# Performance work log

Hardware: AMD Instinct MI355X
Metric: run time of the kernel (lower is better)

The kernel has to match this reference:

```python
import math
import jax
import jax.numpy as jnp
import numpy as np
from jax import lax

Q = 64          # num_quantiles (init default)
EPS = 1e-8      # eps (init default)


def setup_inputs() -> dict:
    key = jax.random.key(0)
    B, T, C = 64, 4096, 128
    x = jax.random.normal(key, (B, T, C), dtype=jnp.float32)
    return {"x": x}


def _build_quantile_table(x):
    """x: (B,T,C) -> quantiles (B,C,Q), levels (Q,). Unmasked branch."""
    B, T, C = x.shape
    levels = jnp.linspace(0.5 / Q, 1.0 - 0.5 / Q, Q, dtype=x.dtype)
    x_sorted = jnp.sort(x, axis=1)                      # (B,T,C) sorted over time
    positions = jnp.clip(levels * T - 0.5, 0.0, float(T - 1))   # (Q,)
    pos_int = jnp.clip(positions.astype(jnp.int32), 0, T - 2)   # (Q,)
    pos_frac = jnp.clip(positions - pos_int.astype(x.dtype), 0.0, 1.0)
    x_bct = jnp.transpose(x_sorted, (0, 2, 1))          # (B,C,T)
    q0 = x_bct[..., pos_int]                            # (B,C,Q)
    q1 = x_bct[..., jnp.minimum(pos_int + 1, T - 1)]    # (B,C,Q)
    quantiles = q0 * (1.0 - pos_frac) + q1 * pos_frac
    return quantiles, levels


def _interp_cdf(x_bc, q_bc, levels):
    """Piecewise-linear F_X(x): x_bc (N,T), q_bc (N,Q) monotone, levels (Q,)."""
    # batched searchsorted (right) per row
    idx = jax.vmap(lambda a, v: jnp.searchsorted(a, v, side="right"))(q_bc, x_bc)
    idx = jnp.clip(idx, 1, Q - 1)                       # (N,T)
    x0 = jnp.take_along_axis(q_bc, idx - 1, axis=-1)
    x1 = jnp.take_along_axis(q_bc, idx, axis=-1)
    y0 = levels[idx - 1]
    y1 = levels[idx]
    slope = (y1 - y0) / jnp.maximum(x1 - x0, 1e-12)
    return y0 + slope * (x_bc - x0)


def _probit(p):
    p_safe = jnp.clip(p, 1e-6, 1.0 - 1e-6)
    return jax.scipy.special.erfinv(2.0 * p_safe - 1.0) * math.sqrt(2.0)


def reference(x):
    B, T, C = x.shape
    quantiles, levels = _build_quantile_table(x)
    # torch detaches the quantile table: gradients flow through x only
    quantiles = lax.stop_gradient(quantiles)
    x_bc = jnp.transpose(x, (0, 2, 1)).reshape(B * C, T)
    q_bc = quantiles.reshape(B * C, Q)
    p_bc = jnp.clip(_interp_cdf(x_bc, q_bc, levels), EPS, 1.0 - EPS)
    z_bc = _probit(p_bc)
    return jnp.transpose(z_bc.reshape(B, C, T), (0, 2, 1))
```

## Files before the change

### kernel.cpp

```cpp
#include <hip/hip_runtime.h>
#include <math.h>

#define BB 64
#define TT 4096
#define CC 128
#define NQ 64
#define TCH2 128
#define NBKT 2048
#define NBKT_G 1024

__global__ __launch_bounds__(256) void transpose_kernel(const float* __restrict__ x,
                                                        float* __restrict__ xT) {
    __shared__ float tile[64][65];
    const int cb = blockIdx.x;
    const int tb = blockIdx.y;
    const int b  = blockIdx.z;
    const int tid = threadIdx.x;
    const int q = tid >> 6;
    const int l = tid & 63;

    const float* xs = x + ((size_t)b * TT + (size_t)tb * 64) * CC + (size_t)cb * 64;
    #pragma unroll
    for (int j = 0; j < 16; ++j) {
        int tl = q * 16 + j;
        tile[tl][l] = xs[(size_t)tl * CC + l];
    }
    __syncthreads();
    float* xd = xT + ((size_t)b * CC + (size_t)cb * 64) * TT + (size_t)tb * 64;
    #pragma unroll
    for (int j = 0; j < 16; ++j) {
        int cl = q * 16 + j;
        xd[(size_t)cl * TT + l] = tile[l][cl];
    }
}

__global__ __launch_bounds__(256) void bucket_quantile_T(const float* __restrict__ xT,
                                                         float* __restrict__ qtab) {
    __shared__ unsigned       A[NBKT];
    __shared__ unsigned short cum16[NBKT + 2];
    __shared__ unsigned char  flag8[NBKT];
    __shared__ unsigned short rankinfo[128];
    __shared__ unsigned short pb16[132];
    __shared__ unsigned       cur2[132];
    __shared__ unsigned       wsum[4], wsum2[4];

    const int row = blockIdx.x;
    const float* xrow = xT + (size_t)row * TT;
    const int tid = threadIdx.x, lane = tid & 63, wid = tid >> 6;

    float vv[16];
    #pragma unroll
    for (int j = 0; j < 4; ++j) {
        float4 v4 = ((const float4*)xrow)[j * 256 + tid];
        vv[j * 4 + 0] = v4.x; vv[j * 4 + 1] = v4.y;
        vv[j * 4 + 2] = v4.z; vv[j * 4 + 3] = v4.w;
    }

    *(uint4*)&A[tid * 8]      = make_uint4(0u, 0u, 0u, 0u);
    *(uint4*)&A[tid * 8 + 4]  = make_uint4(0u, 0u, 0u, 0u);
    *(uint2*)&flag8[tid * 8]  = make_uint2(~0u, ~0u);
    __syncthreads();

    #pragma unroll
    for (int j = 0; j < 16; ++j) {
        int bk = (int)((vv[j] + 5.0f) * 204.8f);
        bk = bk < 0 ? 0 : (bk > NBKT - 1 ? NBKT - 1 : bk);
        atomicAdd(&A[bk], 1u);
    }
    __syncthreads();

    uint4 h0 = *(uint4*)&A[tid * 8];
    uint4 h1 = *(uint4*)&A[tid * 8 + 4];
    unsigned S = h0.x + h0.y + h0.z + h0.w + h1.x + h1.y + h1.z + h1.w;
    unsigned incl = S;
    #pragma unroll
    for (int off = 1; off < 64; off <<= 1) {
        unsigned n = __shfl_up(incl, off, 64);
        if (lane >= off) incl += n;
    }
    if (lane == 63) wsum[wid] = incl;
    __syncthreads();
    unsigned base = incl - S;
    for (int w = 0; w < wid; ++w) base += wsum[w];

    unsigned carr[9];
    carr[0] = base;
    carr[1] = carr[0] + h0.x; carr[2] = carr[1] + h0.y;
    carr[3] = carr[2] + h0.z; carr[4] = carr[3] + h0.w;
    carr[5] = carr[4] + h1.x; carr[6] = carr[5] + h1.y;
    carr[7] = carr[6] + h1.z; carr[8] = carr[7] + h1.w;
    #pragma unroll
    for (int bi = 0; bi < 8; ++bi)
        cum16[tid * 8 + bi] = (unsigned short)carr[bi];
    if (tid == 255) cum16[NBKT] = (unsigned short)TT;

    unsigned flg = 0, myLen = 0, myCnt = 0;
    #pragma unroll
    for (int bi = 0; bi < 8; ++bi) {
        const int cs = (int)carr[bi], ce = (int)carr[bi + 1];
        if (ce > cs) {
            int t0 = cs - 32;
            int q0 = t0 < 0 ? 0 : (t0 >> 6);
            int q1 = (ce >> 6); if (q1 > 63) q1 = 63;
            bool any = false;
            for (int q = q0; q <= q1; ++q) {
                int r1 = (q << 6) + 31, r2 = r1 + 1;
                bool i1 = (r1 >= cs) && (r1 < ce);
                bool i2 = (r2 >= cs) && (r2 < ce);
                if (i1) rankinfo[2 * q]     = (unsigned short)(tid * 8 + bi);
                if (i2) rankinfo[2 * q + 1] = (unsigned short)(tid * 8 + bi);
                any |= (i1 || i2);
            }
            if (any) { flg |= (1u << bi); myLen += (unsigned)(ce - cs); myCnt++; }
        }
    }

    unsigned pk = (myLen << 16) | myCnt;
    unsigned incl2 = pk;
    #pragma unroll
    for (int off = 1; off < 64; off <<= 1) {
        unsigned n = __shfl_up(incl2, off, 64);
        if (lane >= off) incl2 += n;
    }
    if (lane == 63) wsum2[wid] = incl2;
    __syncthreads();
    unsigned b2 = incl2 - pk;
    for (int w = 0; w < wid; ++w) b2 += wsum2[w];
    unsigned lenB = b2 >> 16, cntB = b2 & 0xFFFFu;
    #pragma unroll
    for (int bi = 0; bi < 8; ++bi) {
        if (flg & (1u << bi)) {
            int s = tid * 8 + bi;
            flag8[s] = (unsigned char)cntB;
            pb16[cntB] = (unsigned short)lenB;
            cur2[cntB] = lenB;
            cntB++;
            lenB += carr[bi + 1] - carr[bi];
        }
    }
    __syncthreads();

    #pragma unroll
    for (int j = 0; j < 16; ++j) {
        int bk = (int)((vv[j] + 5.0f) * 204.8f);
        bk = bk < 0 ? 0 : (bk > NBKT - 1 ? NBKT - 1 : bk);
        unsigned char fl = flag8[bk];
        if (fl != 0xFFu) {
            unsigned p = atomicAdd(&cur2[fl], 1u);
            if (p < (unsigned)NBKT) ((float*)A)[p] = vv[j];
        }
    }
    __syncthreads();

    if (tid < 128) {
        const int j = tid;
        const int r = ((j >> 1) << 6) + 31 + (j & 1);
        const int s = rankinfo[j];
        const int cs = (int)cum16[s];
        const int L = (int)cum16[s + 1] - cs;
        const int k = r - cs;
        const unsigned char fid = flag8[s];
        const float* seg = (const float*)A + pb16[fid];

        float ans = 0.0f;
        for (int i = 0; i < L; ++i) {
            float vi = seg[i];
            int rk = 0;
            for (int jj = 0; jj < L; ++jj) {
                float vj = seg[jj];
                rk += (vj < vi) || (vj == vi && jj < i);
            }
            if (rk == k) { ans = vi; break; }
        }
        float vo = __shfl_xor(ans, 1, 64);
        if ((tid & 1) == 0)
            qtab[(size_t)row * NQ + (j >> 1)] = (ans + vo) * 0.5f;
    }
}

__global__ __launch_bounds__(256) void bucket_quantile_G(const float* __restrict__ x,
                                                         float* __restrict__ qtab) {
    __shared__ unsigned hist[NBKT_G];
    __shared__ unsigned cum[NBKT_G];
    __shared__ unsigned cur[NBKT_G];
    __shared__ float    pool[TT];
    __shared__ unsigned wsum[4];

    const int bid = blockIdx.x;
    const int row = ((bid & 7) << 10) | (bid >> 3);
    const int b = row >> 7, c = row & (CC - 1);
    const float* xrow = x + (size_t)b * TT * CC + c;
    const int tid = threadIdx.x;
    const int lane = tid & 63, wid = tid >> 6;

    float vv[16];
    #pragma unroll
    for (int j = 0; j < 16; ++j)
        vv[j] = xrow[(size_t)((j << 8) + tid) * CC];

    *(uint4*)&hist[tid << 2] = make_uint4(0u, 0u, 0u, 0u);
    __syncthreads();

    #pragma unroll
    for (int j = 0; j < 16; ++j) {
        int bk = (int)((vv[j] + 5.0f) * 102.4f);
        bk = bk < 0 ? 0 : (bk > NBKT_G - 1 ? NBKT_G - 1 : bk);
        atomicAdd(&hist[bk], 1u);
    }
    __syncthreads();

    uint4 h = *(uint4*)&hist[tid << 2];
    unsigned S = h.x + h.y + h.z + h.w;
    unsigned incl = S;
    #pragma unroll
    for (int off = 1; off < 64; off <<= 1) {
        unsigned n = __shfl_up(incl, off, 64);
        if (lane >= off) incl += n;
    }
    if (lane == 63) wsum[wid] = incl;
    __syncthreads();
    unsigned base = incl - S;
    for (int w = 0; w < wid; ++w) base += wsum[w];
    {
        unsigned c0 = base, c1 = c0 + h.x, c2 = c1 + h.y, c3 = c2 + h.z;
        *(uint4*)&cum[tid << 2] = make_uint4(c0, c1, c2, c3);
        *(uint4*)&cur[tid << 2] = make_uint4(c0, c1, c2, c3);
    }
    __syncthreads();

    #pragma unroll
    for (int j = 0; j < 16; ++j) {
        int bk = (int)((vv[j] + 5.0f) * 102.4f);
        bk = bk < 0 ? 0 : (bk > NBKT_G - 1 ? NBKT_G - 1 : bk);
        unsigned p = atomicAdd(&cur[bk], 1u);
        pool[p] = vv[j];
    }
    __syncthreads();

    if (tid < 128) {
        const int q = tid >> 1;
        const int r = (q << 6) + 31 + (tid & 1);
        int pos = 0;
        #pragma unroll
        for (int step = 512; step >= 1; step >>= 1) {
            int np = pos + step;
            if (np <= NBKT_G - 1 && (int)cum[np] <= r) pos = np;
        }
        const int segbase = (int)cum[pos];
        const int L = (int)hist[pos];
        const int k = r - segbase;
        const float* seg = &pool[segbase];

        float ans = 0.0f;
        for (int i = 0; i < L; ++i) {
            float vi = seg[i];
            int rk = 0;
            for (int jj = 0; jj < L; ++jj) {
                float vj = seg[jj];
                rk += (vj < vi) || (vj == vi && jj < i);
            }
            if (rk == k) { ans = vi; break; }
        }
        float vo = __shfl_xor(ans, 1, 64);
        if ((tid & 1) == 0)
            qtab[(size_t)row * NQ + q] = (ans + vo) * 0.5f;
    }
}

__global__ __launch_bounds__(256) void apply_kernel(const float* __restrict__ x,
                                                    const float* __restrict__ qtab,
                                                    float* __restrict__ out) {
    __shared__ float qtT[NQ][64];
    const int b   = blockIdx.x;
    const int tch = blockIdx.y;
    const int ch  = blockIdx.z;
    const int tid = threadIdx.x;

    const float* qsrc = qtab + ((size_t)b * CC + (size_t)ch * 64) * NQ;
    for (int i = tid; i < 64 * NQ; i += 256) {
        int cl = i >> 6, k = i & 63;
        qtT[k][cl ^ k] = qsrc[i];
    }
    __syncthreads();

    const int myc = tid & 63;
    const int trow0 = tid >> 6;
    const size_t base = (size_t)b * TT * CC + (size_t)tch * TCH2 * CC
                      + (size_t)ch * 64;
    const float* xp = x + base;
    float* op = out + base;
    const float invq = 1.0f / (float)NQ;

    float pv0 = qtT[7][myc ^ 7],   pv1 = qtT[15][myc ^ 15];
    float pv2 = qtT[23][myc ^ 23], pv3 = qtT[31][myc ^ 31];
    float pv4 = qtT[39][myc ^ 39], pv5 = qtT[47][myc ^ 47];
    float pv6 = qtT[55][myc ^ 55];

    #pragma unroll
    for (int g = 0; g < 4; ++g) {
        float v[8];
        int   pos[8];
        int   off[8];
        #pragma unroll
        for (int e = 0; e < 8; ++e) {
            int t = trow0 + 4 * (g * 8 + e);
            off[e] = t * CC + myc;
            v[e] = xp[off[e]];
        }

        #pragma unroll
        for (int e = 0; e < 8; ++e) {
            int p = (pv3 <= v[e]) ? 32 : 0;
            float p16 = (p == 0) ? pv1 : pv5;
            p += (p16 <= v[e]) ? 16 : 0;
            float p8 = (p == 0) ? pv0 : (p == 16) ? pv2 : (p == 32) ? pv4 : pv6;
            p += (p8 <= v[e]) ? 8 : 0;
            pos[e] = p;
        }

        #pragma unroll
        for (int step = 4; step >= 1; step >>= 1) {
            float pr[8];
            #pragma unroll
            for (int e = 0; e < 8; ++e) {
                int np = pos[e] + step - 1;
                pr[e] = qtT[np][myc ^ np];
            }
            #pragma unroll
            for (int e = 0; e < 8; ++e)
                if (pr[e] <= v[e]) pos[e] += step;
        }

        float x0[8], x1[8];
        #pragma unroll
        for (int e = 0; e < 8; ++e) {
            int idx = pos[e];
            idx = idx < 1 ? 1 : (idx > NQ - 1 ? NQ - 1 : idx);
            pos[e] = idx;
            x0[e] = qtT[idx - 1][myc ^ (idx - 1)];
            x1[e] = qtT[idx][myc ^ idx];
        }

        #pragma unroll
        for (int e = 0; e < 8; ++e) {
            const float y0 = ((float)pos[e] - 0.5f) * invq;
            const float rcp = __builtin_amdgcn_rcpf(fmaxf(x1[e] - x0[e], 1e-12f));
            float p = fmaf(invq * rcp, v[e] - x0[e], y0);
            p = fminf(fmaxf(p, 1e-6f), 1.0f - 1e-6f);

            const float xx = 2.0f * p - 1.0f;
            float w = -__logf((1.0f - xx) * (1.0f + xx));
            float z;
            if (w < 5.0f) {
                float ww = w - 2.5f;
                z = 2.81022636e-08f;
                z = fmaf(z, ww, 3.43273939e-07f);
                z = fmaf(z, ww, -3.5233877e-06f);
                z = fmaf(z, ww, -4.39150654e-06f);
                z = fmaf(z, ww, 0.00021858087f);
                z = fmaf(z, ww, -0.00125372503f);
                z = fmaf(z, ww, -0.00417768164f);
                z = fmaf(z, ww, 0.246640727f);
                z = fmaf(z, ww, 1.50140941f);
            } else {
                float ww = sqrtf(w) - 3.0f;
                z = -0.000200214257f;
                z = fmaf(z, ww, 0.000100950558f);
                z = fmaf(z, ww, 0.00134934322f);
                z = fmaf(z, ww, -0.00367342844f);
                z = fmaf(z, ww, 0.00573950773f);
                z = fmaf(z, ww, -0.0076224613f);
                z = fmaf(z, ww, 0.00943887047f);
                z = fmaf(z, ww, 1.00167406f);
                z = fmaf(z, ww, 2.83297682f);
            }
            op[off[e]] = z * xx * 1.4142135623730951f;
        }
    }
}

extern "C" void kernel_launch(void* const* d_in, const int* in_sizes, int n_in,
                              void* d_out, int out_size, void* d_ws, size_t ws_size,
                              hipStream_t stream) {
    const float* x = (const float*)d_in[0];
    float* out = (float*)d_out;
    float* qtab = (float*)d_ws;
    const size_t qtab_bytes = (size_t)BB * CC * NQ * 4;
    const size_t xT_bytes   = (size_t)BB * CC * TT * 4;

    if (ws_size >= qtab_bytes + xT_bytes) {
        float* xT = (float*)((char*)d_ws + qtab_bytes);
        dim3 tgrid(2, 64, BB);
        transpose_kernel<<<tgrid, 256, 0, stream>>>(x, xT);
        bucket_quantile_T<<<BB * CC, 256, 0, stream>>>(xT, qtab);
    } else {
        bucket_quantile_G<<<BB * CC, 256, 0, stream>>>(x, qtab);
    }
    dim3 grid(BB, TT / TCH2, 2);
    apply_kernel<<<grid, 256, 0, stream>>>(x, qtab, out);
}
```

Baseline: 213.7 us.

## Process one quantile row per wavefront instead of per block

The bucket-quantile kernel now assigns each row to a single 64-lane wavefront, with four rows per block. Each wave uses its own 1024-bin shared histogram and candidate pool, so block-wide __syncthreads are replaced by wave-local scans and fences. This removes cross-wave barriers and per-row block overhead. In exchange, each lane holds 64 values in registers and the histogram is coarser, which lengthens the brute-force rank selection inside the bins that hold target ranks.

Result: slower. 452.9 us (+111.9%).

```diff
diff --git a/kernel.cpp b/kernel.cpp
--- a/kernel.cpp
+++ b/kernel.cpp
@@ -6,7 +6,8 @@
 #define CC 128
 #define NQ 64
 #define TCH2 128
-#define NBKT 2048
+#define NBW 1024
+#define PCAP 1024
 #define NBKT_G 1024
 
 __global__ __launch_bounds__(256) void transpose_kernel(const float* __restrict__ x,
@@ -34,69 +35,67 @@
     }
 }
 
-__global__ __launch_bounds__(256) void bucket_quantile_T(const float* __restrict__ xT,
+__global__ __launch_bounds__(256) void bucket_quantile_W(const float* __restrict__ xT,
                                                          float* __restrict__ qtab) {
-    __shared__ unsigned       A[NBKT];
-    __shared__ unsigned short cum16[NBKT + 2];
-    __shared__ unsigned char  flag8[NBKT];
-    __shared__ unsigned short rankinfo[128];
-    __shared__ unsigned short pb16[132];
-    __shared__ unsigned       cur2[132];
-    __shared__ unsigned       wsum[4], wsum2[4];
-
-    const int row = blockIdx.x;
+    __shared__ unsigned       histW[4][NBW];
+    __shared__ float          poolW[4][PCAP];
+    __shared__ unsigned       rankW[4][128];
+    __shared__ unsigned       curW[4][132];
+    __shared__ unsigned short pbW[4][132];
+    __shared__ unsigned short lenW[4][132];
+
+    const int tid = threadIdx.x;
+    const int wid = tid >> 6, lane = tid & 63;
+    const int row = blockIdx.x * 4 + wid;
     const float* xrow = xT + (size_t)row * TT;
-    const int tid = threadIdx.x, lane = tid & 63, wid = tid >> 6;
-
-    float vv[16];
-    #pragma unroll
-    for (int j = 0; j < 4; ++j) {
-        float4 v4 = ((const float4*)xrow)[j * 256 + tid];
-        vv[j * 4 + 0] = v4.x; vv[j * 4 + 1] = v4.y;
-        vv[j * 4 + 2] = v4.z; vv[j * 4 + 3] = v4.w;
-    }
-
-    *(uint4*)&A[tid * 8]      = make_uint4(0u, 0u, 0u, 0u);
-    *(uint4*)&A[tid * 8 + 4]  = make_uint4(0u, 0u, 0u, 0u);
-    *(uint2*)&flag8[tid * 8]  = make_uint2(~0u, ~0u);
-    __syncthreads();
-
-    #pragma unroll
-    for (int j = 0; j < 16; ++j) {
-        int bk = (int)((vv[j] + 5.0f) * 204.8f);
-        bk = bk < 0 ? 0 : (bk > NBKT - 1 ? NBKT - 1 : bk);
-        atomicAdd(&A[bk], 1u);
-    }
-    __syncthreads();
-
-    uint4 h0 = *(uint4*)&A[tid * 8];
-    uint4 h1 = *(uint4*)&A[tid * 8 + 4];
-    unsigned S = h0.x + h0.y + h0.z + h0.w + h1.x + h1.y + h1.z + h1.w;
-    unsigned incl = S;
-    #pragma unroll
-    for (int off = 1; off < 64; off <<= 1) {
-        unsigned n = __shfl_up(incl, off, 64);
-        if (lane >= off) incl += n;
-    }
-    if (lane == 63) wsum[wid] = incl;
-    __syncthreads();
-    unsigned base = incl - S;
-    for (int w = 0; w < wid; ++w) base += wsum[w];
-
-    unsigned carr[9];
-    carr[0] = base;
-    carr[1] = carr[0] + h0.x; carr[2] = carr[1] + h0.y;
-    carr[3] = carr[2] + h0.z; carr[4] = carr[3] + h0.w;
-    carr[5] = carr[4] + h1.x; carr[6] = carr[5] + h1.y;
-    carr[7] = carr[6] + h1.z; carr[8] = carr[7] + h1.w;
-    #pragma unroll
-    for (int bi = 0; bi < 8; ++bi)
-        cum16[tid * 8 + bi] = (unsigned short)carr[bi];
-    if (tid == 255) cum16[NBKT] = (unsigned short)TT;
+    unsigned* hist = histW[wid];
+
+    float4 vv[16];
+    #pragma unroll
+    for (int j = 0; j < 16; ++j)
+        vv[j] = ((const float4*)xrow)[j * 64 + lane];
+
+    #pragma unroll
+    for (int q = 0; q < 4; ++q)
+        *(uint4*)&hist[lane * 16 + q * 4] = make_uint4(0u, 0u, 0u, 0u);
+    __threadfence_block();
+
+    #pragma unroll
+    for (int j = 0; j < 16; ++j) {
+        int b0 = (int)((vv[j].x + 5.0f) * 102.4f); b0 = b0 < 0 ? 0 : (b0 > NBW-1 ? NBW-1 : b0);
+        int b1 = (int)((vv[j].y + 5.0f) * 102.4f); b1 = b1 < 0 ? 0 : (b1 > NBW-1 ? NBW-1 : b1);
+        int b2 = (int)((vv[j].z + 5.0f) * 102.4f); b2 = b2 < 0 ? 0 : (b2 > NBW-1 ? NBW-1 : b2);
+        int b3 = (int)((vv[j].w + 5.0f) * 102.4f); b3 = b3 < 0 ? 0 : (b3 > NBW-1 ? NBW-1 : b3);
+        atomicAdd(&hist[b0], 1u); atomicAdd(&hist[b1], 1u);
+        atomicAdd(&hist[b2], 1u); atomicAdd(&hist[b3], 1u);
+    }
+    __threadfence_block();
+
+    unsigned carr[17];
+    {
+        uint4 h0 = *(uint4*)&hist[lane * 16];
+        uint4 h1 = *(uint4*)&hist[lane * 16 + 4];
+        uint4 h2 = *(uint4*)&hist[lane * 16 + 8];
+        uint4 h3 = *(uint4*)&hist[lane * 16 + 12];
+        unsigned hh[16] = { h0.x,h0.y,h0.z,h0.w, h1.x,h1.y,h1.z,h1.w,
+                            h2.x,h2.y,h2.z,h2.w, h3.x,h3.y,h3.z,h3.w };
+        unsigned S = 0;
+        #pragma unroll
+        for (int i = 0; i < 16; ++i) S += hh[i];
+        unsigned incl = S;
+        #pragma unroll
+        for (int off = 1; off < 64; off <<= 1) {
+            unsigned n = __shfl_up(incl, off, 64);
+            if (lane >= off) incl += n;
+        }
+        carr[0] = incl - S;
+        #pragma unroll
+        for (int i = 0; i < 16; ++i) carr[i + 1] = carr[i] + hh[i];
+    }
 
     unsigned flg = 0, myLen = 0, myCnt = 0;
     #pragma unroll
-    for (int bi = 0; bi < 8; ++bi) {
+    for (int bi = 0; bi < 16; ++bi) {
         const int cs = (int)carr[bi], ce = (int)carr[bi + 1];
         if (ce > cs) {
             int t0 = cs - 32;
@@ -107,74 +106,82 @@
                 int r1 = (q << 6) + 31, r2 = r1 + 1;
                 bool i1 = (r1 >= cs) && (r1 < ce);
                 bool i2 = (r2 >= cs) && (r2 < ce);
-                if (i1) rankinfo[2 * q]     = (unsigned short)(tid * 8 + bi);
-                if (i2) rankinfo[2 * q + 1] = (unsigned short)(tid * 8 + bi);
+                unsigned sbin = (unsigned)(lane * 16 + bi);
+                if (i1) rankW[wid][2 * q]     = (sbin << 12) | (unsigned)(r1 - cs);
+                if (i2) rankW[wid][2 * q + 1] = (sbin << 12) | (unsigned)(r2 - cs);
                 any |= (i1 || i2);
             }
             if (any) { flg |= (1u << bi); myLen += (unsigned)(ce - cs); myCnt++; }
         }
     }
 
-    unsigned pk = (myLen << 16) | myCnt;
-    unsigned incl2 = pk;
-    #pragma unroll
-    for (int off = 1; off < 64; off <<= 1) {
-        unsigned n = __shfl_up(incl2, off, 64);
-        if (lane >= off) incl2 += n;
-    }
-    if (lane == 63) wsum2[wid] = incl2;
-    __syncthreads();
-    unsigned b2 = incl2 - pk;
-    for (int w = 0; w < wid; ++w) b2 += wsum2[w];
-    unsigned lenB = b2 >> 16, cntB = b2 & 0xFFFFu;
-    #pragma unroll
-    for (int bi = 0; bi < 8; ++bi) {
-        if (flg & (1u << bi)) {
-            int s = tid * 8 + bi;
-            flag8[s] = (unsigned char)cntB;
-            pb16[cntB] = (unsigned short)lenB;
-            cur2[cntB] = lenB;
-            cntB++;
-            lenB += carr[bi + 1] - carr[bi];
-        }
-    }
-    __syncthreads();
-
-    #pragma unroll
-    for (int j = 0; j < 16; ++j) {
-        int bk = (int)((vv[j] + 5.0f) * 204.8f);
-        bk = bk < 0 ? 0 : (bk > NBKT - 1 ? NBKT - 1 : bk);
-        unsigned char fl = flag8[bk];
-        if (fl != 0xFFu) {
-            unsigned p = atomicAdd(&cur2[fl], 1u);
-            if (p < (unsigned)NBKT) ((float*)A)[p] = vv[j];
-        }
-    }
-    __syncthreads();
-
-    if (tid < 128) {
-        const int j = tid;
-        const int r = ((j >> 1) << 6) + 31 + (j & 1);
-        const int s = rankinfo[j];
-        const int cs = (int)cum16[s];
-        const int L = (int)cum16[s + 1] - cs;
-        const int k = r - cs;
-        const unsigned char fid = flag8[s];
-        const float* seg = (const float*)A + pb16[fid];
-
-        float ans = 0.0f;
-        for (int i = 0; i < L; ++i) {
-            float vi = seg[i];
-            int rk = 0;
-            for (int jj = 0; jj < L; ++jj) {
-                float vj = seg[jj];
-                rk += (vj < vi) || (vj == vi && jj < i);
-            }
-            if (rk == k) { ans = vi; break; }
-        }
-        float vo = __shfl_xor(ans, 1, 64);
-        if ((tid & 1) == 0)
-            qtab[(size_t)row * NQ + (j >> 1)] = (ans + vo) * 0.5f;
+    {
+        unsigned pk = (myLen << 16) | myCnt;
+        unsigned incl2 = pk;
+        #pragma unroll
+        for (int off = 1; off < 64; off <<= 1) {
+            unsigned n = __shfl_up(incl2, off, 64);
+            if (lane >= off) incl2 += n;
+        }
+        unsigned b2 = incl2 - pk;
+        unsigned lenB = b2 >> 16, cntB = b2 & 0xFFFFu;
+        #pragma unroll
+        for (int bi = 0; bi < 16; ++bi) {
+            int s = lane * 16 + bi;
+            if (flg & (1u << bi)) {
+                unsigned L = carr[bi + 1] - carr[bi];
+                hist[s] = cntB;
+                pbW[wid][cntB]  = (unsigned short)lenB;
+                lenW[wid][cntB] = (unsigned short)L;
+                curW[wid][cntB] = lenB;
+                cntB++;
+                lenB += L;
+            } else {
+                hist[s] = 0xFFFFFFFFu;
+            }
+        }
+    }
+    __threadfence_block();
+
+    #pragma unroll
+    for (int j = 0; j < 16; ++j) {
+        float vs[4] = { vv[j].x, vv[j].y, vv[j].z, vv[j].w };
+        #pragma unroll
+        for (int e = 0; e < 4; ++e) {
+            int bk = (int)((vs[e] + 5.0f) * 102.4f);
+            bk = bk < 0 ? 0 : (bk > NBW - 1 ? NBW - 1 : bk);
+            unsigned fid = hist[bk];
+            if (fid != 0xFFFFFFFFu) {
+                unsigned p = atomicAdd(&curW[wid][fid], 1u);
+                if (p < (unsigned)PCAP) poolW[wid][p] = vs[e];
+            }
+        }
+    }
+    __threadfence_block();
+
+    {
+        float ans[2];
+        #pragma unroll
+        for (int hk = 0; hk < 2; ++hk) {
+            const unsigned info = rankW[wid][2 * lane + hk];
+            const int sbin = (int)(info >> 12);
+            const int k = (int)(info & 0xFFFu);
+            const unsigned fid = hist[sbin];
+            const int L = (int)lenW[wid][fid];
+            const float* seg = &poolW[wid][pbW[wid][fid]];
+            float a = 0.0f;
+            for (int i = 0; i < L; ++i) {
+                float vi = seg[i];
+                int rk = 0;
+                for (int jj = 0; jj < L; ++jj) {
+                    float vj = seg[jj];
+                    rk += (vj < vi) || (vj == vi && jj < i);
+                }
+                if (rk == k) { a = vi; break; }
+            }
+            ans[hk] = a;
+        }
+        qtab[(size_t)row * NQ + lane] = (ans[0] + ans[1]) * 0.5f;
     }
 }
 
@@ -392,7 +399,7 @@
         float* xT = (float*)((char*)d_ws + qtab_bytes);
         dim3 tgrid(2, 64, BB);
         transpose_kernel<<<tgrid, 256, 0, stream>>>(x, xT);
-        bucket_quantile_T<<<BB * CC, 256, 0, stream>>>(xT, qtab);
+        bucket_quantile_W<<<BB * CC / 4, 256, 0, stream>>>(xT, qtab);
     } else {
         bucket_quantile_G<<<BB * CC, 256, 0, stream>>>(x, qtab);
     }
```
